# Kernel tuning notes

Hardware: AMD Instinct MI355X
Metric: run time of the kernel (lower is better)

The kernel has to match this reference:

```python
import jax, jax.numpy as jnp
import numpy as np

B, N, D, H = 2, 2048, 1024, 16
DK = D // H
SCALE = DK ** -0.5


def setup_inputs() -> dict:
    key = jax.random.key(0)
    ks = jax.random.split(key, 11)
    s = D ** -0.5
    return {
        "q": jax.random.normal(ks[0], (B, N, D), jnp.float32),
        "k": jax.random.normal(ks[1], (B, N, D), jnp.float32),
        "v": jax.random.normal(ks[2], (B, N, D), jnp.float32),
        "Wq": jax.random.normal(ks[3], (D, D), jnp.float32) * s,
        "bq": jnp.zeros((D,), jnp.float32),
        "Wk": jax.random.normal(ks[4], (D, D), jnp.float32) * s,
        "bk": jnp.zeros((D,), jnp.float32),
        "Wv": jax.random.normal(ks[5], (D, D), jnp.float32) * s,
        "bv": jnp.zeros((D,), jnp.float32),
        "Wo": jax.random.normal(ks[6], (D, D), jnp.float32) * s,
        "bo": jnp.zeros((D,), jnp.float32),
    }


def _split_heads(x):
    # [b, n, h*d] -> [b, h, n, d]
    b, n, _ = x.shape
    return x.reshape(b, n, H, DK).transpose(0, 2, 1, 3)


def reference(q, k, v, Wq, bq, Wk, bk, Wv, bv, Wo, bo):
    qh = _split_heads(q @ Wq.T + bq)
    kh = _split_heads(k @ Wk.T + bk)
    vh = _split_heads(v @ Wv.T + bv)
    dots = jnp.einsum('bhid,bhjd->bhij', qh, kh) * SCALE
    attn = jax.nn.softmax(dots, axis=-1)
    out = jnp.einsum('bhij,bhjd->bhid', attn, vh)
    out = out.transpose(0, 2, 1, 3).reshape(q.shape[0], q.shape[1], D)
    return out @ Wo.T + bo
```

## Files before the change

kernel.cpp:

```cpp
#include <hip/hip_runtime.h>
#include <hip/hip_bf16.h>
#include <cstdint>
#include <cstddef>

#define BB 2
#define NN 2048
#define DD 1024
#define HH 16
#define DKK 64
#define SCALE 0.125f
#define LOG2E 1.4426950408889634f

typedef __bf16 bf16;
typedef __bf16 bf16x4 __attribute__((ext_vector_type(4)));
typedef __bf16 bf16x8 __attribute__((ext_vector_type(8)));
typedef float f32x4 __attribute__((ext_vector_type(4)));
typedef short s16x4 __attribute__((ext_vector_type(4)));

#define GLD(gp, lp)                                                            \
  __builtin_amdgcn_global_load_lds(                                            \
      (const __attribute__((address_space(1))) void*)(gp),                     \
      (__attribute__((address_space(3))) void*)(lp), 16, 0, 0)

struct CvtArgs { const float* s[7]; bf16* d[7]; int n[7]; };

__global__ void k_cvt(CvtArgs a) {
  const int seg = blockIdx.y;
  const float* __restrict__ s = a.s[seg];
  bf16* __restrict__ d = a.d[seg];
  int i = (blockIdx.x * 256 + threadIdx.x) * 8;
  if (i >= a.n[seg]) return;
  float4 f0 = *(const float4*)(s + i);
  float4 f1 = *(const float4*)(s + i + 4);
  bf16x8 o;
  o[0] = (bf16)f0.x; o[1] = (bf16)f0.y; o[2] = (bf16)f0.z; o[3] = (bf16)f0.w;
  o[4] = (bf16)f1.x; o[5] = (bf16)f1.y; o[6] = (bf16)f1.z; o[7] = (bf16)f1.w;
  *(bf16x8*)(d + i) = o;
}

template <int BN>
__device__ __forceinline__ void gemm_body(
    const bf16* __restrict__ A, const bf16* __restrict__ W,
    const float* __restrict__ bias, bf16* __restrict__ outB,
    float* __restrict__ outF, int mode, float oscale, int m0, int n0) {
  const int K = 1024;
  constexpr int NI = BN / 32;
  constexpr int BI = BN * 8 / 256;
  __shared__ bf16 lA[128 * 64];
  __shared__ bf16 lB[BN * 64];
  const int t = threadIdx.x;
  const int lane = t & 63, quad = lane >> 4, l16 = lane & 15, w = t >> 6;
  const int wm = (w >> 1) * 64, wn = (w & 1) * (BN / 2);

  f32x4 acc[4][NI] = {};

  const bf16* gA[4]; const bf16* gB[BI];
#pragma unroll
  for (int i4 = 0; i4 < 4; i4++) {
    int i = i4 * 256 + t;
    int r = i >> 3, c = (i & 7) ^ (r & 7);
    gA[i4] = A + (size_t)(m0 + r) * K + c * 8;
  }
#pragma unroll
  for (int i4 = 0; i4 < BI; i4++) {
    int i = i4 * 256 + t;
    int r = i >> 3, c = (i & 7) ^ (r & 7);
    gB[i4] = W + (size_t)(n0 + r) * K + c * 8;
  }

  for (int kb = 0; kb < K; kb += 64) {
    __syncthreads();
#pragma unroll
    for (int i4 = 0; i4 < 4; i4++) GLD(gA[i4] + kb, lA + (i4 * 256 + t) * 8);
#pragma unroll
    for (int i4 = 0; i4 < BI; i4++) GLD(gB[i4] + kb, lB + (i4 * 256 + t) * 8);
    __syncthreads();

#pragma unroll
    for (int kb2 = 0; kb2 < 2; kb2++) {
      bf16x8 af[4], bfr[NI];
      const int ch = ((kb2 * 4 + quad) ^ (l16 & 7)) * 8;
#pragma unroll
      for (int i = 0; i < 4; i++)
        af[i] = *(const bf16x8*)(lA + (wm + i * 16 + l16) * 64 + ch);
#pragma unroll
      for (int i = 0; i < NI; i++)
        bfr[i] = *(const bf16x8*)(lB + (wn + i * 16 + l16) * 64 + ch);
#pragma unroll
      for (int mi = 0; mi < 4; mi++)
#pragma unroll
        for (int ni = 0; ni < NI; ni++)
          acc[mi][ni] = __builtin_amdgcn_mfma_f32_16x16x32_bf16(
              af[mi], bfr[ni], acc[mi][ni], 0, 0, 0);
    }
  }

#pragma unroll
  for (int mi = 0; mi < 4; mi++) {
#pragma unroll
    for (int ni = 0; ni < NI; ni++) {
#pragma unroll
      for (int r = 0; r < 4; r++) {
        int gm = m0 + wm + mi * 16 + quad * 4 + r;
        int gn = n0 + wn + ni * 16 + l16;
        float v = (acc[mi][ni][r] + bias[gn]) * oscale;
        if (mode == 3) {
          outF[(size_t)gm * 1024 + gn] = v;
        } else {
          int b = gm >> 11, row = gm & 2047;
          int h = gn >> 6, dk = gn & 63;
          if (mode == 2)
            outB[((size_t)(b * HH + h) * DKK + dk) * NN + row] = (bf16)v;
          else
            outB[((size_t)(b * HH + h) * NN + row) * DKK + dk] = (bf16)v;
        }
      }
    }
  }
}

struct QkvArgs {
  const bf16* A; const bf16* W; const float* b[3]; bf16* o[3]; float sc0;
};

__global__ __launch_bounds__(256, 3) void k_qkv(QkvArgs g) {
  const int z = blockIdx.z;
  gemm_body<128>(g.A + (size_t)z * 4194304, g.W + (size_t)z * 1048576,
                 g.b[z], g.o[z], nullptr, z == 2 ? 2 : 0,
                 z == 0 ? g.sc0 : 1.0f, blockIdx.x * 128, blockIdx.y * 128);
}

__global__ __launch_bounds__(256, 4) void k_oproj(
    const bf16* __restrict__ A, const bf16* __restrict__ W,
    const float* __restrict__ bias, float* __restrict__ out) {
  gemm_body<64>(A, W, bias, nullptr, out, 3, 1.0f, blockIdx.x * 128,
                blockIdx.y * 64);
}

__global__ __launch_bounds__(512, 4) void k_attn(
    const bf16* __restrict__ Qp, const bf16* __restrict__ Kp,
    const bf16* __restrict__ Vt, bf16* __restrict__ Ao) {
  __shared__ bf16 lK[2][128 * 64];
  __shared__ bf16 lV[2][64 * 128];
  const int t = threadIdx.x;
  const int lane = t & 63, quad = lane >> 4, l16 = lane & 15, w = t >> 6;
  const int wq = w & 3;
  const int kh = w >> 2;
  const int bh = blockIdx.x;
  const int qt = blockIdx.y;
  const bf16* Qb = Qp + (size_t)bh * NN * DKK;
  const bf16* Kb = Kp + (size_t)bh * NN * DKK;
  const bf16* Vb = Vt + (size_t)bh * DKK * NN;

  const int qr0 = qt * 128 + wq * 32;
  bf16x8 qf[2][2];
#pragma unroll
  for (int j = 0; j < 2; j++)
#pragma unroll
    for (int kq = 0; kq < 2; kq++)
      qf[j][kq] = *(const bf16x8*)(Qb + (size_t)(qr0 + j * 16 + l16) * DKK +
                                   kq * 32 + quad * 8);

  float lj[2] = {0.f, 0.f};
  f32x4 oaccT[2][4] = {};

  const bf16* gK[2]; const bf16* gV[2];
#pragma unroll
  for (int i2 = 0; i2 < 2; i2++) {
    int i = i2 * 512 + t;
    int rK = i >> 3, cK = (i & 7) ^ (rK & 7);
    gK[i2] = Kb + (size_t)rK * DKK + cK * 8;
    int rV = i >> 4, cV = (i & 15) ^ (rV & 15);
    gV[i2] = Vb + (size_t)rV * NN + cV * 8;
  }
  const int swzK0 = (quad ^ (l16 & 7)) * 8;
  const int swzK1 = ((4 + quad) ^ (l16 & 7)) * 8;

#pragma unroll
  for (int i2 = 0; i2 < 2; i2++) {
    GLD(gK[i2], &lK[0][(i2 * 512 + t) * 8]);
    GLD(gV[i2], &lV[0][(i2 * 512 + t) * 8]);
  }

  int p = 0;
  for (int kt = 0; kt < NN; kt += 128) {
    __syncthreads();
    if (kt + 128 < NN) {
#pragma unroll
      for (int i2 = 0; i2 < 2; i2++) {
        GLD(gK[i2] + (size_t)(kt + 128) * DKK, &lK[p ^ 1][(i2 * 512 + t) * 8]);
        GLD(gV[i2] + (kt + 128), &lV[p ^ 1][(i2 * 512 + t) * 8]);
      }
    }

    f32x4 s[2][4];
#pragma unroll
    for (int tt = 0; tt < 4; tt++) {
      const bf16* kbase = &lK[p][((kh * 4 + tt) * 16 + l16) * 64];
      bf16x8 kf0 = *(const bf16x8*)(kbase + swzK0);
      bf16x8 kf1 = *(const bf16x8*)(kbase + swzK1);
#pragma unroll
      for (int j = 0; j < 2; j++) {
        f32x4 z = {0.f, 0.f, 0.f, 0.f};
        z = __builtin_amdgcn_mfma_f32_16x16x32_bf16(kf0, qf[j][0], z, 0, 0, 0);
        z = __builtin_amdgcn_mfma_f32_16x16x32_bf16(kf1, qf[j][1], z, 0, 0, 0);
        s[j][tt] = z;
      }
    }

    s16x4 pa[2][4];
#pragma unroll
    for (int j = 0; j < 2; j++) {
      float rs = 0.f;
#pragma unroll
      for (int tt = 0; tt < 4; tt++) {
        bf16x4 pb;
#pragma unroll
        for (int r = 0; r < 4; r++) {
          float pe = __builtin_amdgcn_exp2f(s[j][tt][r]);
          rs += pe;
          pb[r] = (bf16)pe;
        }
        pa[j][tt] = __builtin_bit_cast(s16x4, pb);
      }
      lj[j] += rs;
    }

#pragma unroll
    for (int tt = 0; tt < 4; tt++) {
#pragma unroll
      for (int ni = 0; ni < 4; ni++) {
        int rv = ni * 16 + l16;
        int cc = kh * 8 + 2 * tt + (quad >> 1);
        const bf16* vaddr =
            &lV[p][rv * 128 + ((cc ^ l16) * 8) + (quad & 1) * 4];
        s16x4 vb = __builtin_bit_cast(s16x4, *(const bf16x4*)vaddr);
#pragma unroll
        for (int j = 0; j < 2; j++)
          oaccT[j][ni] = __builtin_amdgcn_mfma_f32_16x16x16bf16_1k(
              vb, pa[j][tt], oaccT[j][ni], 0, 0, 0);
      }
    }
    p ^= 1;
  }

  __syncthreads();
  float* redO = (float*)&lK[0][0];
  float* redL = (float*)&lV[0][0];
  if (kh == 1) {
    float* dst = redO + (wq * 64 + lane) * 32;
#pragma unroll
    for (int j = 0; j < 2; j++)
#pragma unroll
      for (int ni = 0; ni < 4; ni++)
        *(f32x4*)(dst + (j * 4 + ni) * 4) = oaccT[j][ni];
    redL[(wq * 64 + lane) * 2 + 0] = lj[0];
    redL[(wq * 64 + lane) * 2 + 1] = lj[1];
  }
  __syncthreads();
  if (kh == 0) {
    const float* src = redO + (wq * 64 + lane) * 32;
#pragma unroll
    for (int j = 0; j < 2; j++)
#pragma unroll
      for (int ni = 0; ni < 4; ni++)
        oaccT[j][ni] += *(const f32x4*)(src + (j * 4 + ni) * 4);
    lj[0] += redL[(wq * 64 + lane) * 2 + 0];
    lj[1] += redL[(wq * 64 + lane) * 2 + 1];

    const int b = bh >> 4, h = bh & 15;
#pragma unroll
    for (int j = 0; j < 2; j++) {
      float l = lj[j];
      l += __shfl_xor(l, 16);
      l += __shfl_xor(l, 32);
      const float inv = 1.0f / l;
      bf16* dst = Ao + ((size_t)(b * NN) + qr0 + j * 16 + l16) * DD +
                  h * DKK + quad * 4;
#pragma unroll
      for (int ni = 0; ni < 4; ni++) {
        bf16x4 ov;
#pragma unroll
        for (int r = 0; r < 4; r++) ov[r] = (bf16)(oaccT[j][ni][r] * inv);
        *(bf16x4*)(dst + ni * 16) = ov;
      }
    }
  }
}

extern "C" void kernel_launch(void* const* d_in, const int* in_sizes, int n_in,
                              void* d_out, int out_size, void* d_ws,
                              size_t ws_size, hipStream_t stream) {
  const float* qin = (const float*)d_in[0];
  const float* kin = (const float*)d_in[1];
  const float* vin = (const float*)d_in[2];
  const float* Wq = (const float*)d_in[3];
  const float* bq = (const float*)d_in[4];
  const float* Wk = (const float*)d_in[5];
  const float* bk = (const float*)d_in[6];
  const float* Wv = (const float*)d_in[7];
  const float* bv = (const float*)d_in[8];
  const float* Wo = (const float*)d_in[9];
  const float* bo = (const float*)d_in[10];
  float* out = (float*)d_out;

  const int MN = BB * NN * DD;
  const int WNel = DD * DD;
  bf16* ws = (bf16*)d_ws;
  bf16* Xb = ws;
  bf16* Wb = Xb + 3 * MN;
  bf16* Qp = Wb + 4 * WNel;
  bf16* Kp = Qp + MN;
  bf16* Vt = Kp + MN;
  bf16* Ao = Xb;

  CvtArgs ca{{qin, kin, vin, Wq, Wk, Wv, Wo},
             {Xb, Xb + MN, Xb + 2 * MN, Wb, Wb + WNel, Wb + 2 * WNel,
              Wb + 3 * WNel},
             {MN, MN, MN, WNel, WNel, WNel, WNel}};
  k_cvt<<<dim3(2048, 7), 256, 0, stream>>>(ca);

  QkvArgs g{Xb, Wb, {bq, bk, bv}, {Qp, Kp, Vt}, SCALE * LOG2E};
  k_qkv<<<dim3(32, 8, 3), 256, 0, stream>>>(g);
  k_attn<<<dim3(32, 16), 512, 0, stream>>>(Qp, Kp, Vt, Ao);
  k_oproj<<<dim3(32, 16), 256, 0, stream>>>(Ao, Wb + 3 * WNel, bo, out);
}
```

Before: 212.7 us.

## Switch attention to 32x32 MFMA tiles and give oproj a dedicated K=128 tiled GEMM

The attention kernel moves from 16x16 MFMA tiles to 32x32 MFMA instructions (32x32x16 for QK^T, 32x32x8 for PV). Each lane now owns one query row, which simplifies the row-sum reduction and cuts the number of MFMA issues and LDS fragment loads. The output projection gets its own kernel that uses a 128-wide K step with a 16-chunk swizzle, halving the barrier/load iterations, and its occupancy hint drops from 4 to 3. In exchange, the larger accumulators raise register pressure and the bigger LDS tiles in oproj raise shared-memory use.

```diff
diff --git a/kernel.cpp b/kernel.cpp
--- a/kernel.cpp
+++ b/kernel.cpp
@@ -15,6 +15,7 @@
 typedef __bf16 bf16x4 __attribute__((ext_vector_type(4)));
 typedef __bf16 bf16x8 __attribute__((ext_vector_type(8)));
 typedef float f32x4 __attribute__((ext_vector_type(4)));
+typedef float f32x16 __attribute__((ext_vector_type(16)));
 typedef short s16x4 __attribute__((ext_vector_type(4)));
 
 #define GLD(gp, lp)                                                            \
@@ -38,33 +39,25 @@
   *(bf16x8*)(d + i) = o;
 }
 
-template <int BN>
 __device__ __forceinline__ void gemm_body(
     const bf16* __restrict__ A, const bf16* __restrict__ W,
-    const float* __restrict__ bias, bf16* __restrict__ outB,
-    float* __restrict__ outF, int mode, float oscale, int m0, int n0) {
+    const float* __restrict__ bias, bf16* __restrict__ outB, int mode,
+    float oscale, int m0, int n0) {
   const int K = 1024;
-  constexpr int NI = BN / 32;
-  constexpr int BI = BN * 8 / 256;
   __shared__ bf16 lA[128 * 64];
-  __shared__ bf16 lB[BN * 64];
+  __shared__ bf16 lB[128 * 64];
   const int t = threadIdx.x;
   const int lane = t & 63, quad = lane >> 4, l16 = lane & 15, w = t >> 6;
-  const int wm = (w >> 1) * 64, wn = (w & 1) * (BN / 2);
-
-  f32x4 acc[4][NI] = {};
-
-  const bf16* gA[4]; const bf16* gB[BI];
+  const int wm = (w >> 1) * 64, wn = (w & 1) * 64;
+
+  f32x4 acc[4][4] = {};
+
+  const bf16* gA[4]; const bf16* gB[4];
 #pragma unroll
   for (int i4 = 0; i4 < 4; i4++) {
     int i = i4 * 256 + t;
     int r = i >> 3, c = (i & 7) ^ (r & 7);
     gA[i4] = A + (size_t)(m0 + r) * K + c * 8;
-  }
-#pragma unroll
-  for (int i4 = 0; i4 < BI; i4++) {
-    int i = i4 * 256 + t;
-    int r = i >> 3, c = (i & 7) ^ (r & 7);
     gB[i4] = W + (size_t)(n0 + r) * K + c * 8;
   }
 
@@ -73,23 +66,22 @@
 #pragma unroll
     for (int i4 = 0; i4 < 4; i4++) GLD(gA[i4] + kb, lA + (i4 * 256 + t) * 8);
 #pragma unroll
-    for (int i4 = 0; i4 < BI; i4++) GLD(gB[i4] + kb, lB + (i4 * 256 + t) * 8);
+    for (int i4 = 0; i4 < 4; i4++) GLD(gB[i4] + kb, lB + (i4 * 256 + t) * 8);
     __syncthreads();
 
 #pragma unroll
     for (int kb2 = 0; kb2 < 2; kb2++) {
-      bf16x8 af[4], bfr[NI];
+      bf16x8 af[4], bfr[4];
       const int ch = ((kb2 * 4 + quad) ^ (l16 & 7)) * 8;
 #pragma unroll
-      for (int i = 0; i < 4; i++)
+      for (int i = 0; i < 4; i++) {
         af[i] = *(const bf16x8*)(lA + (wm + i * 16 + l16) * 64 + ch);
-#pragma unroll
-      for (int i = 0; i < NI; i++)
         bfr[i] = *(const bf16x8*)(lB + (wn + i * 16 + l16) * 64 + ch);
+      }
 #pragma unroll
       for (int mi = 0; mi < 4; mi++)
 #pragma unroll
-        for (int ni = 0; ni < NI; ni++)
+        for (int ni = 0; ni < 4; ni++)
           acc[mi][ni] = __builtin_amdgcn_mfma_f32_16x16x32_bf16(
               af[mi], bfr[ni], acc[mi][ni], 0, 0, 0);
     }
@@ -98,22 +90,18 @@
 #pragma unroll
   for (int mi = 0; mi < 4; mi++) {
 #pragma unroll
-    for (int ni = 0; ni < NI; ni++) {
+    for (int ni = 0; ni < 4; ni++) {
 #pragma unroll
       for (int r = 0; r < 4; r++) {
         int gm = m0 + wm + mi * 16 + quad * 4 + r;
         int gn = n0 + wn + ni * 16 + l16;
         float v = (acc[mi][ni][r] + bias[gn]) * oscale;
-        if (mode == 3) {
-          outF[(size_t)gm * 1024 + gn] = v;
-        } else {
-          int b = gm >> 11, row = gm & 2047;
-          int h = gn >> 6, dk = gn & 63;
-          if (mode == 2)
-            outB[((size_t)(b * HH + h) * DKK + dk) * NN + row] = (bf16)v;
-          else
-            outB[((size_t)(b * HH + h) * NN + row) * DKK + dk] = (bf16)v;
-        }
+        int b = gm >> 11, row = gm & 2047;
+        int h = gn >> 6, dk = gn & 63;
+        if (mode == 2)
+          outB[((size_t)(b * HH + h) * DKK + dk) * NN + row] = (bf16)v;
+        else
+          outB[((size_t)(b * HH + h) * NN + row) * DKK + dk] = (bf16)v;
       }
     }
   }
@@ -125,16 +113,75 @@
 
 __global__ __launch_bounds__(256, 3) void k_qkv(QkvArgs g) {
   const int z = blockIdx.z;
-  gemm_body<128>(g.A + (size_t)z * 4194304, g.W + (size_t)z * 1048576,
-                 g.b[z], g.o[z], nullptr, z == 2 ? 2 : 0,
-                 z == 0 ? g.sc0 : 1.0f, blockIdx.x * 128, blockIdx.y * 128);
-}
-
-__global__ __launch_bounds__(256, 4) void k_oproj(
+  gemm_body(g.A + (size_t)z * 4194304, g.W + (size_t)z * 1048576, g.b[z],
+            g.o[z], z == 2 ? 2 : 0, z == 0 ? g.sc0 : 1.0f, blockIdx.x * 128,
+            blockIdx.y * 128);
+}
+
+__global__ __launch_bounds__(256, 3) void k_oproj(
     const bf16* __restrict__ A, const bf16* __restrict__ W,
     const float* __restrict__ bias, float* __restrict__ out) {
-  gemm_body<64>(A, W, bias, nullptr, out, 3, 1.0f, blockIdx.x * 128,
-                blockIdx.y * 64);
+  const int K = 1024;
+  __shared__ bf16 lA[128 * 128];
+  __shared__ bf16 lB[64 * 128];
+  const int t = threadIdx.x;
+  const int lane = t & 63, quad = lane >> 4, l16 = lane & 15, w = t >> 6;
+  const int wm = (w >> 1) * 64, wn = (w & 1) * 32;
+  const int m0 = blockIdx.x * 128, n0 = blockIdx.y * 64;
+
+  f32x4 acc[4][2] = {};
+
+  const bf16* gA[8]; const bf16* gB[4];
+#pragma unroll
+  for (int i8 = 0; i8 < 8; i8++) {
+    int i = i8 * 256 + t;
+    int r = i >> 4, c = (i & 15) ^ (r & 15);
+    gA[i8] = A + (size_t)(m0 + r) * K + c * 8;
+  }
+#pragma unroll
+  for (int i4 = 0; i4 < 4; i4++) {
+    int i = i4 * 256 + t;
+    int r = i >> 4, c = (i & 15) ^ (r & 15);
+    gB[i4] = W + (size_t)(n0 + r) * K + c * 8;
+  }
+
+  for (int kb = 0; kb < K; kb += 128) {
+    __syncthreads();
+#pragma unroll
+    for (int i8 = 0; i8 < 8; i8++) GLD(gA[i8] + kb, lA + (i8 * 256 + t) * 8);
+#pragma unroll
+    for (int i4 = 0; i4 < 4; i4++) GLD(gB[i4] + kb, lB + (i4 * 256 + t) * 8);
+    __syncthreads();
+
+#pragma unroll
+    for (int kb2 = 0; kb2 < 4; kb2++) {
+      bf16x8 af[4], bfr[2];
+      const int ch = ((kb2 * 4 + quad) ^ (l16 & 15)) * 8;
+#pragma unroll
+      for (int i = 0; i < 4; i++)
+        af[i] = *(const bf16x8*)(lA + (wm + i * 16 + l16) * 128 + ch);
+#pragma unroll
+      for (int i = 0; i < 2; i++)
+        bfr[i] = *(const bf16x8*)(lB + (wn + i * 16 + l16) * 128 + ch);
+#pragma unroll
+      for (int mi = 0; mi < 4; mi++)
+#pragma unroll
+        for (int ni = 0; ni < 2; ni++)
+          acc[mi][ni] = __builtin_amdgcn_mfma_f32_16x16x32_bf16(
+              af[mi], bfr[ni], acc[mi][ni], 0, 0, 0);
+    }
+  }
+
+#pragma unroll
+  for (int mi = 0; mi < 4; mi++)
+#pragma unroll
+    for (int ni = 0; ni < 2; ni++)
+#pragma unroll
+      for (int r = 0; r < 4; r++) {
+        int gm = m0 + wm + mi * 16 + quad * 4 + r;
+        int gn = n0 + wn + ni * 16 + l16;
+        out[(size_t)gm * 1024 + gn] = acc[mi][ni][r] + bias[gn];
+      }
 }
 
 __global__ __launch_bounds__(512, 4) void k_attn(
@@ -143,7 +190,7 @@
   __shared__ bf16 lK[2][128 * 64];
   __shared__ bf16 lV[2][64 * 128];
   const int t = threadIdx.x;
-  const int lane = t & 63, quad = lane >> 4, l16 = lane & 15, w = t >> 6;
+  const int lane = t & 63, l32 = lane & 31, hi = lane >> 5, w = t >> 6;
   const int wq = w & 3;
   const int kh = w >> 2;
   const int bh = blockIdx.x;
@@ -152,17 +199,14 @@
   const bf16* Kb = Kp + (size_t)bh * NN * DKK;
   const bf16* Vb = Vt + (size_t)bh * DKK * NN;
 
-  const int qr0 = qt * 128 + wq * 32;
-  bf16x8 qf[2][2];
-#pragma unroll
-  for (int j = 0; j < 2; j++)
-#pragma unroll
-    for (int kq = 0; kq < 2; kq++)
-      qf[j][kq] = *(const bf16x8*)(Qb + (size_t)(qr0 + j * 16 + l16) * DKK +
-                                   kq * 32 + quad * 8);
-
-  float lj[2] = {0.f, 0.f};
-  f32x4 oaccT[2][4] = {};
+  const int qr = qt * 128 + wq * 32 + l32;
+  bf16x8 qf[4];
+#pragma unroll
+  for (int kblk = 0; kblk < 4; kblk++)
+    qf[kblk] = *(const bf16x8*)(Qb + (size_t)qr * DKK + kblk * 16 + hi * 8);
+
+  float lj = 0.f;
+  f32x16 oaccT[2] = {};
 
   const bf16* gK[2]; const bf16* gV[2];
 #pragma unroll
@@ -173,8 +217,6 @@
     int rV = i >> 4, cV = (i & 15) ^ (rV & 15);
     gV[i2] = Vb + (size_t)rV * NN + cV * 8;
   }
-  const int swzK0 = (quad ^ (l16 & 7)) * 8;
-  const int swzK1 = ((4 + quad) ^ (l16 & 7)) * 8;
 
 #pragma unroll
   for (int i2 = 0; i2 < 2; i2++) {
@@ -193,98 +235,87 @@
       }
     }
 
-    f32x4 s[2][4];
-#pragma unroll
-    for (int tt = 0; tt < 4; tt++) {
-      const bf16* kbase = &lK[p][((kh * 4 + tt) * 16 + l16) * 64];
-      bf16x8 kf0 = *(const bf16x8*)(kbase + swzK0);
-      bf16x8 kf1 = *(const bf16x8*)(kbase + swzK1);
-#pragma unroll
-      for (int j = 0; j < 2; j++) {
-        f32x4 z = {0.f, 0.f, 0.f, 0.f};
-        z = __builtin_amdgcn_mfma_f32_16x16x32_bf16(kf0, qf[j][0], z, 0, 0, 0);
-        z = __builtin_amdgcn_mfma_f32_16x16x32_bf16(kf1, qf[j][1], z, 0, 0, 0);
-        s[j][tt] = z;
-      }
+    f32x16 s[2];
+#pragma unroll
+    for (int kk = 0; kk < 2; kk++) {
+      const int keyrow = kh * 64 + kk * 32 + l32;
+      const bf16* kbase = &lK[p][keyrow * 64];
+      f32x16 z = {};
+#pragma unroll
+      for (int kblk = 0; kblk < 4; kblk++) {
+        const int cc = kblk * 2 + hi;
+        bf16x8 kf = *(const bf16x8*)(kbase + ((cc ^ (keyrow & 7)) * 8));
+        z = __builtin_amdgcn_mfma_f32_32x32x16_bf16(kf, qf[kblk], z, 0, 0, 0);
+      }
+      s[kk] = z;
     }
 
     s16x4 pa[2][4];
-#pragma unroll
-    for (int j = 0; j < 2; j++) {
-      float rs = 0.f;
-#pragma unroll
-      for (int tt = 0; tt < 4; tt++) {
+    float rs = 0.f;
+#pragma unroll
+    for (int kk = 0; kk < 2; kk++)
+#pragma unroll
+      for (int b = 0; b < 4; b++) {
         bf16x4 pb;
 #pragma unroll
-        for (int r = 0; r < 4; r++) {
-          float pe = __builtin_amdgcn_exp2f(s[j][tt][r]);
+        for (int j = 0; j < 4; j++) {
+          float pe = __builtin_amdgcn_exp2f(s[kk][4 * b + j]);
           rs += pe;
-          pb[r] = (bf16)pe;
+          pb[j] = (bf16)pe;
         }
-        pa[j][tt] = __builtin_bit_cast(s16x4, pb);
-      }
-      lj[j] += rs;
-    }
-
-#pragma unroll
-    for (int tt = 0; tt < 4; tt++) {
-#pragma unroll
-      for (int ni = 0; ni < 4; ni++) {
-        int rv = ni * 16 + l16;
-        int cc = kh * 8 + 2 * tt + (quad >> 1);
-        const bf16* vaddr =
-            &lV[p][rv * 128 + ((cc ^ l16) * 8) + (quad & 1) * 4];
-        s16x4 vb = __builtin_bit_cast(s16x4, *(const bf16x4*)vaddr);
-#pragma unroll
-        for (int j = 0; j < 2; j++)
-          oaccT[j][ni] = __builtin_amdgcn_mfma_f32_16x16x16bf16_1k(
-              vb, pa[j][tt], oaccT[j][ni], 0, 0, 0);
-      }
+        pa[kk][b] = __builtin_bit_cast(s16x4, pb);
+      }
+    lj += rs;
+
+#pragma unroll
+    for (int nt = 0; nt < 2; nt++) {
+      const int rv = nt * 32 + l32;
+      const bf16* rowbase = &lV[p][rv * 128];
+#pragma unroll
+      for (int kk = 0; kk < 2; kk++)
+#pragma unroll
+        for (int b = 0; b < 4; b++) {
+          const int cc = kh * 8 + kk * 4 + b;
+          s16x4 vb = __builtin_bit_cast(
+              s16x4,
+              *(const bf16x4*)(rowbase + ((cc ^ (rv & 15)) * 8) + hi * 4));
+          oaccT[nt] = __builtin_amdgcn_mfma_f32_32x32x8bf16_1k(
+              vb, pa[kk][b], oaccT[nt], 0, 0, 0);
+        }
     }
     p ^= 1;
   }
+
+  lj += __shfl_xor(lj, 32);
 
   __syncthreads();
   float* redO = (float*)&lK[0][0];
   float* redL = (float*)&lV[0][0];
   if (kh == 1) {
     float* dst = redO + (wq * 64 + lane) * 32;
-#pragma unroll
-    for (int j = 0; j < 2; j++)
-#pragma unroll
-      for (int ni = 0; ni < 4; ni++)
-        *(f32x4*)(dst + (j * 4 + ni) * 4) = oaccT[j][ni];
-    redL[(wq * 64 + lane) * 2 + 0] = lj[0];
-    redL[(wq * 64 + lane) * 2 + 1] = lj[1];
+    *(f32x16*)(dst) = oaccT[0];
+    *(f32x16*)(dst + 16) = oaccT[1];
+    redL[wq * 64 + lane] = lj;
   }
   __syncthreads();
   if (kh == 0) {
     const float* src = redO + (wq * 64 + lane) * 32;
-#pragma unroll
-    for (int j = 0; j < 2; j++)
-#pragma unroll
-      for (int ni = 0; ni < 4; ni++)
-        oaccT[j][ni] += *(const f32x4*)(src + (j * 4 + ni) * 4);
-    lj[0] += redL[(wq * 64 + lane) * 2 + 0];
-    lj[1] += redL[(wq * 64 + lane) * 2 + 1];
-
+    oaccT[0] += *(const f32x16*)(src);
+    oaccT[1] += *(const f32x16*)(src + 16);
+    lj += redL[wq * 64 + lane];
+
+    const float inv = 1.0f / lj;
     const int b = bh >> 4, h = bh & 15;
-#pragma unroll
-    for (int j = 0; j < 2; j++) {
-      float l = lj[j];
-      l += __shfl_xor(l, 16);
-      l += __shfl_xor(l, 32);
-      const float inv = 1.0f / l;
-      bf16* dst = Ao + ((size_t)(b * NN) + qr0 + j * 16 + l16) * DD +
-                  h * DKK + quad * 4;
-#pragma unroll
-      for (int ni = 0; ni < 4; ni++) {
+    bf16* dst = Ao + ((size_t)(b * NN) + qr) * DD + h * DKK + hi * 4;
+#pragma unroll
+    for (int nt = 0; nt < 2; nt++)
+#pragma unroll
+      for (int g = 0; g < 4; g++) {
         bf16x4 ov;
 #pragma unroll
-        for (int r = 0; r < 4; r++) ov[r] = (bf16)(oaccT[j][ni][r] * inv);
-        *(bf16x4*)(dst + ni * 16) = ov;
-      }
-    }
+        for (int j = 0; j < 4; j++) ov[j] = (bf16)(oaccT[nt][4 * g + j] * inv);
+        *(bf16x4*)(dst + nt * 32 + g * 8) = ov;
+      }
   }
 }
 
```

Measured after the change: 232.3 us. 9.2% more time.
